# Optimization experiments

Hardware: AMD Instinct MI355X
Metric: run time of the kernel (lower is better)

The kernel has to match this reference:

```python
import jax, jax.numpy as jnp
import numpy as np
import math

N_NODES = 20000
N_EDGES = 320000
MUL = 64          # multiplicity of each irrep block
N_BASIS = 10
N_HID = 100
W_NUMEL = 4 * MUL  # 4 'uvu' instructions, v=1


def setup_inputs() -> dict:
    key = jax.random.key(0)
    ks = jax.random.split(key, 16)
    node_input = jax.random.normal(ks[0], (N_NODES, 4 * MUL), dtype=jnp.float32)  # 64x0e + 64x1o -> 64 + 192
    node_attr = jnp.ones((N_NODES, 1), dtype=jnp.float32)
    node_deg = jax.random.randint(ks[1], (N_NODES, 1), 1, 33).astype(jnp.float32)
    edge_src = jax.random.randint(ks[2], (N_EDGES,), 0, N_NODES)
    edge_dst = jax.random.randint(ks[3], (N_EDGES,), 0, N_NODES)
    edge_attr = jax.random.normal(ks[4], (N_EDGES, 4), dtype=jnp.float32)  # sh: 1x0e + 1x1o
    edge_length_embedded = jax.random.uniform(ks[5], (N_EDGES, N_BASIS), dtype=jnp.float32)
    # FullyConnectedTensorProduct weights (node_attr is 1x0e -> per-irrep linear mixing)
    W_li0 = jax.random.normal(ks[6], (MUL, MUL), dtype=jnp.float32)
    W_li1 = jax.random.normal(ks[7], (MUL, MUL), dtype=jnp.float32)
    W_lm0 = jax.random.normal(ks[8], (MUL, MUL), dtype=jnp.float32)
    W_lm1 = jax.random.normal(ks[9], (MUL, MUL), dtype=jnp.float32)
    # radial MLP: number_of_basis -> radial_neurons -> weight_numel (no bias, e3nn FullyConnectedNet style)
    W_mlp1 = jax.random.normal(ks[10], (N_BASIS, N_HID), dtype=jnp.float32)
    W_mlp2 = jax.random.normal(ks[11], (N_HID, W_NUMEL), dtype=jnp.float32)
    # linear_output: irreps_mid (128x0e + 128x1o) x 1x0e -> 64x0e + 64x1o
    W_lo0 = jax.random.normal(ks[12], (2 * MUL, MUL), dtype=jnp.float32)
    W_lo1 = jax.random.normal(ks[13], (2 * MUL, MUL), dtype=jnp.float32)
    return dict(node_input=node_input, node_attr=node_attr, node_deg=node_deg,
                edge_attr=edge_attr, edge_length_embedded=edge_length_embedded,
                W_li0=W_li0, W_li1=W_li1, W_lm0=W_lm0, W_lm1=W_lm1,
                W_mlp1=W_mlp1, W_mlp2=W_mlp2, W_lo0=W_lo0, W_lo1=W_lo1,
                edge_src=edge_src, edge_dst=edge_dst)


def _split(x):
    # split 64x0e + 64x1o feature vector into scalar [*,64] and vector [*,64,3] parts
    s = x[..., :MUL]
    v = x[..., MUL:].reshape(x.shape[:-1] + (MUL, 3))
    return s, v


def _fctp(s, v, W0, W1, attr, fan_in):
    # FullyConnectedTensorProduct with 1x0e attr: per-irrep linear, path-normalized
    inv = 1.0 / math.sqrt(fan_in)
    o0 = jnp.einsum('nu,uk->nk', s, W0) * attr * inv
    o1 = jnp.einsum('num,uk->nkm', v, W1) * attr[..., None] * inv
    return o0, o1


def reference(node_input, node_attr, node_deg, edge_attr, edge_length_embedded,
              W_li0, W_li1, W_lm0, W_lm1, W_mlp1, W_mlp2, W_lo0, W_lo1,
              edge_src, edge_dst):
    N = node_input.shape[0]
    x0, x1 = _split(node_input)

    # linear_input then degree pre-normalization
    f0, f1 = _fctp(x0, x1, W_li0, W_li1, node_attr, MUL)
    deg_isqrt = 1.0 / jnp.sqrt(node_deg)            # [N,1]
    f0 = f0 * deg_isqrt
    f1 = f1 * deg_isqrt[..., None]

    # linear_mask (skip path)
    m0, m1 = _fctp(x0, x1, W_lm0, W_lm1, node_attr, MUL)

    # radial MLP -> per-edge tensor-product weights [E, 256]
    h = jax.nn.silu(edge_length_embedded @ W_mlp1 / math.sqrt(N_BASIS))
    ew = (h @ W_mlp2) / math.sqrt(N_HID)
    wa, wb, wc, wd = ew[:, :MUL], ew[:, MUL:2*MUL], ew[:, 2*MUL:3*MUL], ew[:, 3*MUL:]

    # gather source-node features per edge
    g0 = f0[edge_src]                                # [E,64]
    g1 = f1[edge_src]                                # [E,64,3]
    y0 = edge_attr[:, 0]                             # [E]   1x0e
    y1 = edge_attr[:, 1:4]                           # [E,3] 1x1o

    # 'uvu' tensor product paths (block-diagonal equivariant contractions)
    m0a = wa * g0 * y0[:, None]                                        # 0e x 0e -> 0e
    m0b = wb * jnp.einsum('eum,em->eu', g1, y1) / math.sqrt(3.0)       # 1o x 1o -> 0e
    m1a = wc[:, :, None] * g0[:, :, None] * y1[:, None, :]             # 0e x 1o -> 1o
    m1b = wd[:, :, None] * g1 * y0[:, None, None]                      # 1o x 0e -> 1o

    # scatter-sum into destination nodes (irreps_mid = 128x0e + 128x1o)
    s_mid = jax.ops.segment_sum(jnp.concatenate([m0a, m0b], axis=1), edge_dst, num_segments=N)          # [N,128]
    v_mid = jax.ops.segment_sum(jnp.concatenate([m1a, m1b], axis=1), edge_dst, num_segments=N)          # [N,128,3]

    # degree post-normalization
    s_mid = s_mid * deg_isqrt
    v_mid = v_mid * deg_isqrt[..., None]

    # linear_output
    o0, o1 = _fctp(s_mid, v_mid, W_lo0, W_lo1, node_attr, 2 * MUL)

    # masked skip combination; output_mask is all ones here (every out irrep is reachable)
    c_s, c_x = math.sin(math.pi / 8), math.cos(math.pi / 8)
    out0 = c_s * m0 + c_x * o0                       # [N,64]
    out1 = c_s * m1 + c_x * o1                       # [N,64,3]
    return jnp.concatenate([out0, out1.reshape(N, 3 * MUL)], axis=1)  # [N,256]
```

## Files before the change

### kernel.cpp

```cpp
#include <hip/hip_runtime.h>
#include <hip/hip_bf16.h>
#include <math.h>

#define N_NODES 20000
#define N_EDGES 320000

#define INV1   0.31622776601683794f
#define SC2    0.1f
#define IS3    0.5773502691896258f
#define C_S    0.3826834323650898f
#define C_X    0.9238795325112867f
#define INV64  0.125f
#define INVLO  0.08838834764831845f

typedef short     short8 __attribute__((ext_vector_type(8)));
typedef float     f32x4  __attribute__((ext_vector_type(4)));

__device__ __forceinline__ float silu_f(float x) {
    float e = __builtin_amdgcn_exp2f(-1.44269504088896f * x);
    return x * __builtin_amdgcn_rcpf(1.0f + e);
}
__device__ __forceinline__ unsigned short f2bf(float x) {
    __hip_bfloat16 h = __float2bfloat16(x);
    return *reinterpret_cast<unsigned short*>(&h);
}
__device__ __forceinline__ float bf2f(unsigned short u) {
    __hip_bfloat16 h;
    *reinterpret_cast<unsigned short*>(&h) = u;
    return __bfloat162float(h);
}

__global__ __launch_bounds__(256) void k_pre(
    const float* __restrict__ ni, const float* __restrict__ attr,
    const float* __restrict__ deg,
    const float* __restrict__ Wli0, const float* __restrict__ Wli1,
    const float* __restrict__ Wlm0, const float* __restrict__ Wlm1,
    ushort4* __restrict__ fvb, float* __restrict__ out,
    const int* __restrict__ edst, int* __restrict__ hist,
    const float* __restrict__ W2, const float* __restrict__ W1,
    unsigned short* __restrict__ w2t, unsigned short* __restrict__ w1t)
{
    __shared__ float raw[4][256];
    if (blockIdx.x < N_NODES / 4) {
        const int wave = threadIdx.x >> 6;
        const int lane = threadIdx.x & 63;
        const int n = blockIdx.x * 4 + wave;

        const float* row = ni + (size_t)n * 256;
        raw[wave][lane      ] = row[lane      ];
        raw[wave][lane + 64 ] = row[lane + 64 ];
        raw[wave][lane + 128] = row[lane + 128];
        raw[wave][lane + 192] = row[lane + 192];
        __syncthreads();

        float f0 = 0.f, m0 = 0.f;
        float f1x = 0.f, f1y = 0.f, f1z = 0.f;
        float m1x = 0.f, m1y = 0.f, m1z = 0.f;
        #pragma unroll 4
        for (int t = 0; t < 64; ++t) {
            float xs  = raw[wave][t];
            float xv0 = raw[wave][64 + t*3    ];
            float xv1 = raw[wave][64 + t*3 + 1];
            float xv2 = raw[wave][64 + t*3 + 2];
            float a0 = Wli0[t*64 + lane];
            float a1 = Wli1[t*64 + lane];
            float b0 = Wlm0[t*64 + lane];
            float b1 = Wlm1[t*64 + lane];
            f0  += xs  * a0;   m0  += xs  * b0;
            f1x += xv0 * a1;   f1y += xv1 * a1;   f1z += xv2 * a1;
            m1x += xv0 * b1;   m1y += xv1 * b1;   m1z += xv2 * b1;
        }

        const float a   = attr[n] * INV64;
        const float dis = 1.0f / sqrtf(deg[n]);
        const float fa  = a * dis;

        ushort4 pk;
        pk.x = f2bf(f0  * fa);
        pk.y = f2bf(f1x * fa);
        pk.z = f2bf(f1y * fa);
        pk.w = f2bf(f1z * fa);
        fvb[(size_t)n * 64 + lane] = pk;

        float* orow = out + (size_t)n * 256;
        orow[lane] = C_S * m0 * a;
        orow[64 + lane*3    ] = C_S * m1x * a;
        orow[64 + lane*3 + 1] = C_S * m1y * a;
        orow[64 + lane*3 + 2] = C_S * m1z * a;
    } else if (blockIdx.x < N_NODES / 4 + N_EDGES / 256) {
        const int e = (blockIdx.x - N_NODES / 4) * 256 + threadIdx.x;
        atomicAdd(&hist[edst[e]], 1);
    } else {
        const int i = (blockIdx.x - N_NODES / 4 - N_EDGES / 256) * 256
                    + threadIdx.x;
        if (i < 32768) {
            const int n = i >> 7, k = i & 127;
            w2t[i] = (k < 100) ? f2bf(W2[k*256 + n] * SC2) : (unsigned short)0;
        } else if (i < 32768 + 3584) {
            const int j = i - 32768;
            const int n = j >> 5, k = j & 31;
            w1t[j] = (k < 10 && n < 100) ? f2bf(W1[k*100 + n] * INV1)
                                         : (unsigned short)0;
        }
    }
}

__global__ __launch_bounds__(1024) void k_scan(const int* __restrict__ hist,
                                               int* __restrict__ starts,
                                               int* __restrict__ cursor) {
    __shared__ int part[1024];
    const int t = threadIdx.x;
    const int C = 20;
    const int base = t * C;
    int s = 0;
    for (int i = 0; i < C; ++i) {
        const int idx = base + i;
        if (idx < N_NODES) s += hist[idx];
    }
    part[t] = s;
    __syncthreads();
    for (int off = 1; off < 1024; off <<= 1) {
        int v = (t >= off) ? part[t - off] : 0;
        __syncthreads();
        part[t] += v;
        __syncthreads();
    }
    int run = part[t] - s;
    for (int i = 0; i < C; ++i) {
        const int idx = base + i;
        if (idx < N_NODES) {
            starts[idx] = run;
            cursor[idx] = run;
            run += hist[idx];
        }
    }
    if (t == 1023) starts[N_NODES] = N_EDGES;
}

__global__ __launch_bounds__(256) void k_scatter(
    const int* __restrict__ esrc, const int* __restrict__ edst,
    const float4* __restrict__ eattr4, const float* __restrict__ elen,
    int* __restrict__ cursor, int* __restrict__ esrc_s,
    float4* __restrict__ eattrs, unsigned short* __restrict__ elen_sb)
{
    const int e = blockIdx.x * 256 + threadIdx.x;
    if (e < N_EDGES) {
        const int p = atomicAdd(&cursor[edst[e]], 1);
        esrc_s[p] = esrc[e];
        eattrs[p] = eattr4[e];
        const float* el = elen + (size_t)e * 10;
        unsigned short v[32];
        #pragma unroll
        for (int b = 0; b < 10; ++b) v[b] = f2bf(el[b]);
        #pragma unroll
        for (int b = 10; b < 32; ++b) v[b] = 0;
        short8* dst = (short8*)(elen_sb + (size_t)p * 32);
        #pragma unroll
        for (int s = 0; s < 4; ++s) {
            short8 pk;
            #pragma unroll
            for (int j = 0; j < 8; ++j) pk[j] = (short)v[s*8 + j];
            dst[s] = pk;
        }
    }
}

__device__ __forceinline__ void p2_ldB(const unsigned short* __restrict__ w2t,
                                       int ntA, int m15, int q,
                                       short8* BA, short8* BB)
{
    const unsigned short* bpA = w2t + ((size_t)(ntA*16 + m15) << 7);
    const unsigned short* bpB = w2t + ((size_t)((ntA + 4)*16 + m15) << 7);
    #pragma unroll
    for (int s = 0; s < 4; ++s) {
        BA[s] = *(const short8*)(bpA + s*32 + q*8);
        BB[s] = *(const short8*)(bpB + s*32 + q*8);
    }
}

__device__ __forceinline__ void p2_mfma_store(
    const short8* A0, const short8* A1,
    const short8* BA, const short8* BB,
    unsigned int* __restrict__ dstp,
    int e0, int eb, int m15, int q, int nt4)
{
    f32x4 ca0 = {0.f,0.f,0.f,0.f}, ca1 = {0.f,0.f,0.f,0.f};
    f32x4 cb0 = {0.f,0.f,0.f,0.f}, cb1 = {0.f,0.f,0.f,0.f};
    #pragma unroll
    for (int s = 0; s < 4; ++s) {
        ca0 = __builtin_amdgcn_mfma_f32_16x16x32_bf16(BA[s], A0[s], ca0, 0, 0, 0);
        ca1 = __builtin_amdgcn_mfma_f32_16x16x32_bf16(BA[s], A1[s], ca1, 0, 0, 0);
        cb0 = __builtin_amdgcn_mfma_f32_16x16x32_bf16(BB[s], A0[s], cb0, 0, 0, 0);
        cb1 = __builtin_amdgcn_mfma_f32_16x16x32_bf16(BB[s], A1[s], cb1, 0, 0, 0);
    }
    uint4 U0, U1;
    U0.x = (unsigned int)f2bf(ca0[0]) | ((unsigned int)f2bf(cb0[0]) << 16);
    U0.y = (unsigned int)f2bf(ca0[1]) | ((unsigned int)f2bf(cb0[1]) << 16);
    U0.z = (unsigned int)f2bf(ca0[2]) | ((unsigned int)f2bf(cb0[2]) << 16);
    U0.w = (unsigned int)f2bf(ca0[3]) | ((unsigned int)f2bf(cb0[3]) << 16);
    U1.x = (unsigned int)f2bf(ca1[0]) | ((unsigned int)f2bf(cb1[0]) << 16);
    U1.y = (unsigned int)f2bf(ca1[1]) | ((unsigned int)f2bf(cb1[1]) << 16);
    U1.z = (unsigned int)f2bf(ca1[2]) | ((unsigned int)f2bf(cb1[2]) << 16);
    U1.w = (unsigned int)f2bf(ca1[3]) | ((unsigned int)f2bf(cb1[3]) << 16);
    *(uint4*)(dstp + (size_t)(e0 + eb      + m15)*64 + nt4*16 + q*4) = U0;
    *(uint4*)(dstp + (size_t)(e0 + eb + 16 + m15)*64 + nt4*16 + q*4) = U1;
}

__global__ __launch_bounds__(256, 4) void k_mlp(
    const unsigned short* __restrict__ elen_sb,
    const unsigned short* __restrict__ w1t,
    const unsigned short* __restrict__ w2t,
    unsigned int* __restrict__ ewAB,
    unsigned int* __restrict__ ewCD)
{
    __shared__ unsigned short Hs[128 * 136];
    const int t    = threadIdx.x;
    const int w    = t >> 6;
    const int lane = t & 63;
    const int m15  = lane & 15;
    const int q    = lane >> 4;
    const int eb   = w * 32;
    const int e0   = blockIdx.x * 128;

    short8 xa0 = *(const short8*)(elen_sb + (size_t)(e0 + eb      + m15)*32 + q*8);
    short8 xa1 = *(const short8*)(elen_sb + (size_t)(e0 + eb + 16 + m15)*32 + q*8);

    short8 bw[7];
    #pragma unroll
    for (int nt = 0; nt < 7; ++nt)
        bw[nt] = *(const short8*)(w1t + (nt*16 + m15)*32 + q*8);

    short8 Ba[4], Bb[4], Ca[4], Cb[4];
    p2_ldB(w2t, 0 , m15, q, Ba, Bb);

    {
        const int r = eb + (lane >> 1);
        const int c = 112 + (lane & 1) * 8;
        short8 z = {0,0,0,0,0,0,0,0};
        *(short8*)&Hs[r*136 + c] = z;
    }

    #pragma unroll
    for (int nt = 0; nt < 7; ++nt) {
        f32x4 z4 = {0.f, 0.f, 0.f, 0.f};
        f32x4 h0 = __builtin_amdgcn_mfma_f32_16x16x32_bf16(bw[nt], xa0, z4, 0, 0, 0);
        f32x4 h1 = __builtin_amdgcn_mfma_f32_16x16x32_bf16(bw[nt], xa1, z4, 0, 0, 0);
        uint2 d0, d1;
        d0.x = (unsigned int)f2bf(silu_f(h0[0])) | ((unsigned int)f2bf(silu_f(h0[1])) << 16);
        d0.y = (unsigned int)f2bf(silu_f(h0[2])) | ((unsigned int)f2bf(silu_f(h0[3])) << 16);
        d1.x = (unsigned int)f2bf(silu_f(h1[0])) | ((unsigned int)f2bf(silu_f(h1[1])) << 16);
        d1.y = (unsigned int)f2bf(silu_f(h1[2])) | ((unsigned int)f2bf(silu_f(h1[3])) << 16);
        *(uint2*)&Hs[(eb      + m15)*136 + nt*16 + q*4] = d0;
        *(uint2*)&Hs[(eb + 16 + m15)*136 + nt*16 + q*4] = d1;
    }

    short8 A0[4], A1[4];
    #pragma unroll
    for (int s = 0; s < 4; ++s) {
        A0[s] = *(const short8*)&Hs[(eb      + m15)*136 + s*32 + q*8];
        A1[s] = *(const short8*)&Hs[(eb + 16 + m15)*136 + s*32 + q*8];
    }

    #pragma unroll
    for (int ii = 0; ii < 4; ++ii) {
        const int i0 = 2*ii, i1 = 2*ii + 1;
        const int ntA1 = ((i1 >> 2) * 8) + (i1 & 3);
        p2_ldB(w2t, ntA1, m15, q, Ca, Cb);
        {
            unsigned int* dst0 = (i0 >> 2) ? ewCD : ewAB;
            p2_mfma_store(A0, A1, Ba, Bb, dst0, e0, eb, m15, q, i0 & 3);
        }
        if (ii < 3) {
            const int i2 = i0 + 2;
            const int ntA2 = ((i2 >> 2) * 8) + (i2 & 3);
            p2_ldB(w2t, ntA2, m15, q, Ba, Bb);
        }
        {
            unsigned int* dst1 = (i1 >> 2) ? ewCD : ewAB;
            p2_mfma_store(A0, A1, Ca, Cb, dst1, e0, eb, m15, q, i1 & 3);
        }
    }
}

__global__ __launch_bounds__(256) void k_gather(
    const int* __restrict__ starts, const int* __restrict__ esrc_s,
    const float4* __restrict__ eattrs,
    const unsigned int* __restrict__ ewAB,
    const unsigned int* __restrict__ ewCD,
    const ushort4* __restrict__ fvb,
    const float* __restrict__ attr, const float* __restrict__ deg,
    const float* __restrict__ Wlo0, const float* __restrict__ Wlo1,
    float* __restrict__ out)
{
    __shared__ float sm[4][512];
    const int wave = threadIdx.x >> 6;
    const int lane = threadIdx.x & 63;
    const int n = blockIdx.x * 4 + wave;

    const int beg = starts[n], end = starts[n + 1];
    float sA=0.f, sB=0.f;
    float vA0=0.f, vA1=0.f, vA2=0.f;
    float vB0=0.f, vB1=0.f, vB2=0.f;

    for (int base = beg; base < end; base += 64) {
        const int cnt = min(64, end - base);
        int    srcv = 0;
        float4 eav  = make_float4(0.f, 0.f, 0.f, 0.f);
        if (lane < cnt) {
            srcv = esrc_s[base + lane];
            eav  = eattrs[base + lane];
        }
        #pragma unroll 2
        for (int j = 0; j < cnt; ++j) {
            const int   src = __shfl(srcv, j);
            const float y0  = __shfl(eav.x, j);
            const float y10 = __shfl(eav.y, j);
            const float y11 = __shfl(eav.z, j);
            const float y12 = __shfl(eav.w, j);

            const unsigned int uab = ewAB[(size_t)(base + j)*64 + lane];
            const unsigned int ucd = ewCD[(size_t)(base + j)*64 + lane];
            const float wa = bf2f((unsigned short)(uab & 0xFFFFu));
            const float wb = bf2f((unsigned short)(uab >> 16));
            const float wc = bf2f((unsigned short)(ucd & 0xFFFFu));
            const float wd = bf2f((unsigned short)(ucd >> 16));

            const ushort4 g4 = fvb[(size_t)src * 64 + lane];
            const float g0  = bf2f(g4.x);
            const float g10 = bf2f(g4.y);
            const float g11 = bf2f(g4.z);
            const float g12 = bf2f(g4.w);

            const float dotv = g10*y10 + g11*y11 + g12*y12;
            sA += wa * g0 * y0;
            sB += wb * dotv;
            const float t0 = wc * g0;
            vA0 += t0 * y10;  vA1 += t0 * y11;  vA2 += t0 * y12;
            const float t1 = wd * y0;
            vB0 += t1 * g10;  vB1 += t1 * g11;  vB2 += t1 * g12;
        }
    }

    const float dis = 1.0f / sqrtf(deg[n]);
    sm[wave][lane            ] = sA * dis;
    sm[wave][64  + lane      ] = sB * IS3 * dis;
    sm[wave][128 + lane      ] = vA0 * dis;
    sm[wave][128 + 64 + lane ] = vB0 * dis;
    sm[wave][256 + lane      ] = vA1 * dis;
    sm[wave][256 + 64 + lane ] = vB1 * dis;
    sm[wave][384 + lane      ] = vA2 * dis;
    sm[wave][384 + 64 + lane ] = vB2 * dis;
    __syncthreads();

    float o0=0.f, o1x=0.f, o1y=0.f, o1z=0.f;
    #pragma unroll 4
    for (int c = 0; c < 128; ++c) {
        const float w0 = Wlo0[c*64 + lane];
        const float w1 = Wlo1[c*64 + lane];
        o0  += sm[wave][c]         * w0;
        o1x += sm[wave][128 + c]   * w1;
        o1y += sm[wave][256 + c]   * w1;
        o1z += sm[wave][384 + c]   * w1;
    }

    const float a = attr[n] * INVLO;
    float* orow = out + (size_t)n * 256;
    orow[lane] += C_X * o0 * a;
    orow[64 + lane*3    ] += C_X * o1x * a;
    orow[64 + lane*3 + 1] += C_X * o1y * a;
    orow[64 + lane*3 + 2] += C_X * o1z * a;
}

__global__ __launch_bounds__(256) void k_node_in_legacy(
    const float* __restrict__ ni, const float* __restrict__ attr,
    const float* __restrict__ deg,
    const float* __restrict__ Wli0, const float* __restrict__ Wli1,
    const float* __restrict__ Wlm0, const float* __restrict__ Wlm1,
    float* __restrict__ f, float* __restrict__ out)
{
    __shared__ float raw[4][256];
    const int wave = threadIdx.x >> 6;
    const int lane = threadIdx.x & 63;
    const int n = blockIdx.x * 4 + wave;

    const float* row = ni + (size_t)n * 256;
    raw[wave][lane      ] = row[lane      ];
    raw[wave][lane + 64 ] = row[lane + 64 ];
    raw[wave][lane + 128] = row[lane + 128];
    raw[wave][lane + 192] = row[lane + 192];
    __syncthreads();

    float f0 = 0.f, m0 = 0.f;
    float f1x = 0.f, f1y = 0.f, f1z = 0.f;
    float m1x = 0.f, m1y = 0.f, m1z = 0.f;
    for (int t = 0; t < 64; ++t) {
        float xs  = raw[wave][t];
        float xv0 = raw[wave][64 + t*3    ];
        float xv1 = raw[wave][64 + t*3 + 1];
        float xv2 = raw[wave][64 + t*3 + 2];
        float a0 = Wli0[t*64 + lane];
        float a1 = Wli1[t*64 + lane];
        float b0 = Wlm0[t*64 + lane];
        float b1 = Wlm1[t*64 + lane];
        f0  += xs  * a0;   m0  += xs  * b0;
        f1x += xv0 * a1;   f1y += xv1 * a1;   f1z += xv2 * a1;
        m1x += xv0 * b1;   m1y += xv1 * b1;   m1z += xv2 * b1;
    }

    const float a   = attr[n] * INV64;
    const float dis = 1.0f / sqrtf(deg[n]);
    const float fa  = a * dis;

    float* fr = f + (size_t)n * 256;
    fr[lane      ] = f0  * fa;
    fr[64  + lane] = f1x * fa;
    fr[128 + lane] = f1y * fa;
    fr[192 + lane] = f1z * fa;

    float* orow = out + (size_t)n * 256;
    orow[lane] = C_S * m0 * a;
    orow[64 + lane*3    ] = C_S * m1x * a;
    orow[64 + lane*3 + 1] = C_S * m1y * a;
    orow[64 + lane*3 + 2] = C_S * m1z * a;
}

__global__ __launch_bounds__(256) void k_edge_legacy(
    const float* __restrict__ eattr, const float* __restrict__ elen,
    const float* __restrict__ W1, const float* __restrict__ W2,
    const int* __restrict__ esrc, const int* __restrict__ edst,
    const float* __restrict__ f, float* __restrict__ acc)
{
    __shared__ float hsh[4][104];
    const int wave = threadIdx.x >> 6;
    const int lane = threadIdx.x & 63;
    const int e = blockIdx.x * 4 + wave;

    const float* el = elen + (size_t)e * 10;
    float elr[10];
    #pragma unroll
    for (int b = 0; b < 10; ++b) elr[b] = el[b];

    float a1 = 0.f;
    #pragma unroll
    for (int b = 0; b < 10; ++b) a1 += elr[b] * W1[b*100 + lane];
    hsh[wave][lane] = silu_f(a1 * INV1);
    if (lane < 36) {
        float a2 = 0.f;
        #pragma unroll
        for (int b = 0; b < 10; ++b) a2 += elr[b] * W1[b*100 + 64 + lane];
        hsh[wave][64 + lane] = silu_f(a2 * INV1);
    }
    __syncthreads();

    float wa = 0.f, wb = 0.f, wc = 0.f, wd = 0.f;
    for (int j = 0; j < 100; ++j) {
        float hj = hsh[wave][j];
        const float* wr = W2 + j*256;
        wa += hj * wr[lane      ];
        wb += hj * wr[64  + lane];
        wc += hj * wr[128 + lane];
        wd += hj * wr[192 + lane];
    }
    wa *= SC2; wb *= SC2; wc *= SC2; wd *= SC2;

    const int src = esrc[e];
    const int dst = edst[e];
    const float y0  = eattr[e*4 + 0];
    const float y10 = eattr[e*4 + 1];
    const float y11 = eattr[e*4 + 2];
    const float y12 = eattr[e*4 + 3];

    const float* fr = f + (size_t)src * 256;
    const float g0  = fr[lane      ];
    const float g10 = fr[64  + lane];
    const float g11 = fr[128 + lane];
    const float g12 = fr[192 + lane];

    const float dotv = g10*y10 + g11*y11 + g12*y12;

    float* ar = acc + (size_t)dst * 512;
    atomicAdd(ar + lane,                  wa * g0 * y0);
    atomicAdd(ar + 64 + lane,             wb * dotv * IS3);
    atomicAdd(ar + 128 +   0 + lane,      wc * g0 * y10);
    atomicAdd(ar + 128 + 128 + lane,      wc * g0 * y11);
    atomicAdd(ar + 128 + 256 + lane,      wc * g0 * y12);
    atomicAdd(ar + 128 +   0 + 64 + lane, wd * g10 * y0);
    atomicAdd(ar + 128 + 128 + 64 + lane, wd * g11 * y0);
    atomicAdd(ar + 128 + 256 + 64 + lane, wd * g12 * y0);
}

__global__ __launch_bounds__(256) void k_node_out_legacy(
    const float* __restrict__ acc, const float* __restrict__ attr,
    const float* __restrict__ deg, const float* __restrict__ Wlo0,
    const float* __restrict__ Wlo1, float* __restrict__ out)
{
    __shared__ float sm[4][512];
    const int wave = threadIdx.x >> 6;
    const int lane = threadIdx.x & 63;
    const int n = blockIdx.x * 4 + wave;

    const float dis = 1.0f / sqrtf(deg[n]);
    const float* ar = acc + (size_t)n * 512;
    for (int i = lane; i < 512; i += 64) sm[wave][i] = ar[i] * dis;
    __syncthreads();

    float o0 = 0.f, o1x = 0.f, o1y = 0.f, o1z = 0.f;
    for (int c = 0; c < 128; ++c) {
        float w0 = Wlo0[c*64 + lane];
        float w1 = Wlo1[c*64 + lane];
        o0  += sm[wave][c]        * w0;
        o1x += sm[wave][128 + c]  * w1;
        o1y += sm[wave][256 + c]  * w1;
        o1z += sm[wave][384 + c]  * w1;
    }

    const float a = attr[n] * INVLO;
    float* orow = out + (size_t)n * 256;
    orow[lane] += C_X * o0 * a;
    orow[64 + lane*3    ] += C_X * o1x * a;
    orow[64 + lane*3 + 1] += C_X * o1y * a;
    orow[64 + lane*3 + 2] += C_X * o1z * a;
}

extern "C" void kernel_launch(void* const* d_in, const int* in_sizes, int n_in,
                              void* d_out, int out_size, void* d_ws, size_t ws_size,
                              hipStream_t stream) {
    const float* ni    = (const float*)d_in[0];
    const float* attr  = (const float*)d_in[1];
    const float* deg   = (const float*)d_in[2];
    const float* eattr = (const float*)d_in[3];
    const float* elen  = (const float*)d_in[4];
    const float* Wli0  = (const float*)d_in[5];
    const float* Wli1  = (const float*)d_in[6];
    const float* Wlm0  = (const float*)d_in[7];
    const float* Wlm1  = (const float*)d_in[8];
    const float* Wm1   = (const float*)d_in[9];
    const float* Wm2   = (const float*)d_in[10];
    const float* Wlo0  = (const float*)d_in[11];
    const float* Wlo1  = (const float*)d_in[12];
    const int*   esrc  = (const int*)d_in[13];
    const int*   edst  = (const int*)d_in[14];

    float* out = (float*)d_out;

    char* wsb = (char*)d_ws;
    size_t off = 0;
    ushort4* fvb = (ushort4*)(wsb + off);               off += (size_t)N_NODES * 64 * 8;
    unsigned int* ewAB = (unsigned int*)(wsb + off);    off += (size_t)N_EDGES * 64 * 4;
    unsigned int* ewCD = (unsigned int*)(wsb + off);    off += (size_t)N_EDGES * 64 * 4;
    unsigned short* elen_sb = (unsigned short*)(wsb + off); off += (size_t)N_EDGES * 32 * 2;
    float4* eattrs = (float4*)(wsb + off);              off += (size_t)N_EDGES * 16;
    int* esrc_s = (int*)(wsb + off);                    off += (size_t)N_EDGES * 4;
    unsigned short* w2t = (unsigned short*)(wsb + off); off += 32768 * 2;
    unsigned short* w1t = (unsigned short*)(wsb + off); off += 3584 * 2;
    int* starts = (int*)(wsb + off);                    off += (size_t)(N_NODES + 4) * 4;
    int* hist   = (int*)(wsb + off);                    off += (size_t)N_NODES * 4;
    int* cursor = (int*)(wsb + off);                    off += (size_t)N_NODES * 4;
    const size_t need_fast = off;

    if (ws_size >= need_fast) {
        hipMemsetAsync(hist, 0, (size_t)N_NODES * sizeof(int), stream);
        k_pre    <<<N_NODES / 4 + N_EDGES / 256 + 144, 256, 0, stream>>>(
                     ni, attr, deg, Wli0, Wli1, Wlm0, Wlm1, fvb, out,
                     edst, hist, Wm2, Wm1, w2t, w1t);
        k_scan   <<<1, 1024, 0, stream>>>(hist, starts, cursor);
        k_scatter<<<N_EDGES / 256, 256, 0, stream>>>(esrc, edst,
                                                     (const float4*)eattr, elen,
                                                     cursor, esrc_s, eattrs, elen_sb);
        k_mlp    <<<N_EDGES / 128, 256, 0, stream>>>(elen_sb, w1t, w2t, ewAB, ewCD);
        k_gather <<<N_NODES / 4, 256, 0, stream>>>(starts, esrc_s, eattrs,
                                                   ewAB, ewCD, fvb, attr, deg,
                                                   Wlo0, Wlo1, out);
    } else {
        float* f   = (float*)d_ws;
        float* acc = f + (size_t)N_NODES * 256;
        hipMemsetAsync(acc, 0, (size_t)N_NODES * 512 * sizeof(float), stream);
        k_node_in_legacy<<<N_NODES / 4, 256, 0, stream>>>(ni, attr, deg, Wli0, Wli1,
                                                          Wlm0, Wlm1, f, out);
        k_edge_legacy<<<N_EDGES / 4, 256, 0, stream>>>(eattr, elen, Wm1, Wm2,
                                                       esrc, edst, f, acc);
        k_node_out_legacy<<<N_NODES / 4, 256, 0, stream>>>(acc, attr, deg,
                                                           Wlo0, Wlo1, out);
    }
}
```

Measured before the change: 396.6 us.

## Merge scatter and edge MLP into one launch, MLP in original edge order

The scatter kernel and the edge MLP kernel become one launch: the first blocks do the CSR scatter of src and attrs plus a new edge index, and the rest run the MLP directly from raw fp32 edge-length inputs in original edge order. This removes the intermediate bf16 elen buffer, its write and read, and a kernel boundary. In exchange the gather kernel now reads the per-edge weights (ewAB/ewCD) through an indirection, randomly instead of sequentially. That could hurt locality on the largest stream (about 160 MB of edge weights).

Result: faster. 385.7 us (-2.7%).

```diff
diff --git a/kernel.cpp b/kernel.cpp
--- a/kernel.cpp
+++ b/kernel.cpp
@@ -137,32 +137,23 @@
     if (t == 1023) starts[N_NODES] = N_EDGES;
 }
 
-__global__ __launch_bounds__(256) void k_scatter(
-    const int* __restrict__ esrc, const int* __restrict__ edst,
-    const float4* __restrict__ eattr4, const float* __restrict__ elen,
-    int* __restrict__ cursor, int* __restrict__ esrc_s,
-    float4* __restrict__ eattrs, unsigned short* __restrict__ elen_sb)
-{
-    const int e = blockIdx.x * 256 + threadIdx.x;
-    if (e < N_EDGES) {
-        const int p = atomicAdd(&cursor[edst[e]], 1);
-        esrc_s[p] = esrc[e];
-        eattrs[p] = eattr4[e];
-        const float* el = elen + (size_t)e * 10;
-        unsigned short v[32];
-        #pragma unroll
-        for (int b = 0; b < 10; ++b) v[b] = f2bf(el[b]);
-        #pragma unroll
-        for (int b = 10; b < 32; ++b) v[b] = 0;
-        short8* dst = (short8*)(elen_sb + (size_t)p * 32);
-        #pragma unroll
-        for (int s = 0; s < 4; ++s) {
-            short8 pk;
-            #pragma unroll
-            for (int j = 0; j < 8; ++j) pk[j] = (short)v[s*8 + j];
-            dst[s] = pk;
-        }
-    }
+
+__device__ __forceinline__ short8 ld_elen8(const float* __restrict__ elen,
+                                           int e, int q)
+{
+    const float* er = elen + (size_t)e * 10 + q * 8;
+    float v0 = er[0], v1 = er[1];
+    float v2 = 0.f, v3 = 0.f, v4 = 0.f, v5 = 0.f, v6 = 0.f, v7 = 0.f;
+    if (q == 0) {
+        v2 = er[2]; v3 = er[3]; v4 = er[4];
+        v5 = er[5]; v6 = er[6]; v7 = er[7];
+    }
+    short8 r;
+    r[0] = (short)f2bf(v0); r[1] = (short)f2bf(v1);
+    r[2] = (short)f2bf(v2); r[3] = (short)f2bf(v3);
+    r[4] = (short)f2bf(v4); r[5] = (short)f2bf(v5);
+    r[6] = (short)f2bf(v6); r[7] = (short)f2bf(v7);
+    return r;
 }
 
 __device__ __forceinline__ void p2_ldB(const unsigned short* __restrict__ w2t,
@@ -206,24 +197,37 @@
     *(uint4*)(dstp + (size_t)(e0 + eb + 16 + m15)*64 + nt4*16 + q*4) = U1;
 }
 
-__global__ __launch_bounds__(256, 4) void k_mlp(
-    const unsigned short* __restrict__ elen_sb,
+__global__ __launch_bounds__(256, 4) void k_mid(
+    const int* __restrict__ esrc, const int* __restrict__ edst,
+    const float4* __restrict__ eattr4, const float* __restrict__ elen,
+    int* __restrict__ cursor, int* __restrict__ esrc_s,
+    int* __restrict__ eidx_s, float4* __restrict__ eattrs,
     const unsigned short* __restrict__ w1t,
     const unsigned short* __restrict__ w2t,
     unsigned int* __restrict__ ewAB,
     unsigned int* __restrict__ ewCD)
 {
     __shared__ unsigned short Hs[128 * 136];
+
+    if (blockIdx.x < N_EDGES / 256) {
+        const int e = blockIdx.x * 256 + threadIdx.x;
+        const int p = atomicAdd(&cursor[edst[e]], 1);
+        esrc_s[p] = esrc[e];
+        eidx_s[p] = e;
+        eattrs[p] = eattr4[e];
+        return;
+    }
+
     const int t    = threadIdx.x;
     const int w    = t >> 6;
     const int lane = t & 63;
     const int m15  = lane & 15;
     const int q    = lane >> 4;
     const int eb   = w * 32;
-    const int e0   = blockIdx.x * 128;
-
-    short8 xa0 = *(const short8*)(elen_sb + (size_t)(e0 + eb      + m15)*32 + q*8);
-    short8 xa1 = *(const short8*)(elen_sb + (size_t)(e0 + eb + 16 + m15)*32 + q*8);
+    const int e0   = (blockIdx.x - N_EDGES / 256) * 128;
+
+    short8 xa0 = ld_elen8(elen, e0 + eb      + m15, q);
+    short8 xa1 = ld_elen8(elen, e0 + eb + 16 + m15, q);
 
     short8 bw[7];
     #pragma unroll
@@ -284,6 +288,7 @@
 
 __global__ __launch_bounds__(256) void k_gather(
     const int* __restrict__ starts, const int* __restrict__ esrc_s,
+    const int* __restrict__ eidx_s,
     const float4* __restrict__ eattrs,
     const unsigned int* __restrict__ ewAB,
     const unsigned int* __restrict__ ewCD,
@@ -304,22 +309,24 @@
 
     for (int base = beg; base < end; base += 64) {
         const int cnt = min(64, end - base);
-        int    srcv = 0;
+        int    srcv = 0, eidxv = 0;
         float4 eav  = make_float4(0.f, 0.f, 0.f, 0.f);
         if (lane < cnt) {
-            srcv = esrc_s[base + lane];
-            eav  = eattrs[base + lane];
+            srcv  = esrc_s[base + lane];
+            eidxv = eidx_s[base + lane];
+            eav   = eattrs[base + lane];
         }
         #pragma unroll 2
         for (int j = 0; j < cnt; ++j) {
             const int   src = __shfl(srcv, j);
+            const int   ei  = __shfl(eidxv, j);
             const float y0  = __shfl(eav.x, j);
             const float y10 = __shfl(eav.y, j);
             const float y11 = __shfl(eav.z, j);
             const float y12 = __shfl(eav.w, j);
 
-            const unsigned int uab = ewAB[(size_t)(base + j)*64 + lane];
-            const unsigned int ucd = ewCD[(size_t)(base + j)*64 + lane];
+            const unsigned int uab = ewAB[(size_t)ei*64 + lane];
+            const unsigned int ucd = ewCD[(size_t)ei*64 + lane];
             const float wa = bf2f((unsigned short)(uab & 0xFFFFu));
             const float wb = bf2f((unsigned short)(uab >> 16));
             const float wc = bf2f((unsigned short)(ucd & 0xFFFFu));
@@ -548,9 +555,9 @@
     ushort4* fvb = (ushort4*)(wsb + off);               off += (size_t)N_NODES * 64 * 8;
     unsigned int* ewAB = (unsigned int*)(wsb + off);    off += (size_t)N_EDGES * 64 * 4;
     unsigned int* ewCD = (unsigned int*)(wsb + off);    off += (size_t)N_EDGES * 64 * 4;
-    unsigned short* elen_sb = (unsigned short*)(wsb + off); off += (size_t)N_EDGES * 32 * 2;
     float4* eattrs = (float4*)(wsb + off);              off += (size_t)N_EDGES * 16;
     int* esrc_s = (int*)(wsb + off);                    off += (size_t)N_EDGES * 4;
+    int* eidx_s = (int*)(wsb + off);                    off += (size_t)N_EDGES * 4;
     unsigned short* w2t = (unsigned short*)(wsb + off); off += 32768 * 2;
     unsigned short* w1t = (unsigned short*)(wsb + off); off += 3584 * 2;
     int* starts = (int*)(wsb + off);                    off += (size_t)(N_NODES + 4) * 4;
@@ -564,12 +571,13 @@
                      ni, attr, deg, Wli0, Wli1, Wlm0, Wlm1, fvb, out,
                      edst, hist, Wm2, Wm1, w2t, w1t);
         k_scan   <<<1, 1024, 0, stream>>>(hist, starts, cursor);
-        k_scatter<<<N_EDGES / 256, 256, 0, stream>>>(esrc, edst,
-                                                     (const float4*)eattr, elen,
-                                                     cursor, esrc_s, eattrs, elen_sb);
-        k_mlp    <<<N_EDGES / 128, 256, 0, stream>>>(elen_sb, w1t, w2t, ewAB, ewCD);
-        k_gather <<<N_NODES / 4, 256, 0, stream>>>(starts, esrc_s, eattrs,
-                                                   ewAB, ewCD, fvb, attr, deg,
+        k_mid    <<<N_EDGES / 256 + N_EDGES / 128, 256, 0, stream>>>(
+                     esrc, edst, (const float4*)eattr, elen,
+                     cursor, esrc_s, eidx_s, eattrs,
+                     w1t, w2t, ewAB, ewCD);
+        k_gather <<<N_NODES / 4, 256, 0, stream>>>(starts, esrc_s, eidx_s,
+                                                   eattrs, ewAB, ewCD,
+                                                   fvb, attr, deg,
                                                    Wlo0, Wlo1, out);
     } else {
         float* f   = (float*)d_ws;
```
